# Performance work log

Measured on AMD Instinct MI355X. Metric: run time of the kernel, lower is better.

Reference implementation:

```python
import jax, jax.numpy as jnp
import numpy as np

THRESHOLD = 0.01
TOPK_RATIO = 0.7

def setup_inputs() -> dict:
    key = jax.random.key(0)
    k1, k2, k3, k4, k5 = jax.random.split(key, 5)
    B, N, F, K = 8, 2048, 512, 256
    x = jax.random.normal(k1, (B, N, F), dtype=jnp.float32)
    adj = jax.random.uniform(k2, (B, N, N), dtype=jnp.float32)
    mask = jnp.ones((B, N), dtype=jnp.float32)
    # assign_main = Linear(F->K), ReLU, Linear(K->K)
    W1 = jax.random.normal(k3, (F, K), dtype=jnp.float32) / np.sqrt(F)
    b1 = jnp.zeros((K,), dtype=jnp.float32)
    W2 = jax.random.normal(k4, (K, K), dtype=jnp.float32) / np.sqrt(K)
    b2 = jnp.zeros((K,), dtype=jnp.float32)
    return {"x": x, "adj": adj, "mask": mask, "W1": W1, "b1": b1, "W2": W2, "b2": b2}

def reference(x, adj, mask, W1, b1, W2, b2):
    B, N, Fdim = x.shape
    K = W2.shape[1]
    # soft assignment logits with masked softmax over clusters
    h = jax.nn.relu(jnp.einsum('bnf,fk->bnk', x, W1) + b1)
    logits = jnp.einsum('bnk,kl->bnl', h, W2) + b2            # [B,N,K]
    logits = logits + (-1e9) * (1.0 - mask[..., None])
    S = jax.nn.softmax(logits, axis=-1)                       # [B,N,K]
    # pooled features and pooled adjacency
    pfeat = jnp.einsum('bnk,bnf->bkf', S, x)                  # S^T x -> [B,K,F]
    mid = jnp.einsum('bnm,bmk->bnk', adj, S)                  # adj @ S
    pooled = jnp.einsum('bnk,bnl->bkl', S, mid)               # S^T adj S -> [B,K,K]
    # threshold + top-k sparsify with straight-through estimator
    topk = min(K, int(np.ceil(TOPK_RATIO * K)))
    thr_mask = (pooled >= THRESHOLD).astype(pooled.dtype)
    a_thr = pooled * thr_mask
    _, idx = jax.lax.top_k(a_thr, topk)                       # [B,K,topk]
    bi = jnp.arange(B)[:, None, None]
    ri = jnp.arange(K)[None, :, None]
    fmask = jnp.zeros_like(pooled).at[bi, ri, idx].set(1.0)
    a_sp = pooled * fmask
    a_ste = a_sp + jax.lax.stop_gradient(pooled - a_sp)       # forward == pooled
    # symmetric degree renormalization
    row_sum = a_ste.sum(axis=-1)
    d_inv_sqrt = 1.0 / jnp.sqrt(row_sum + 1e-9)
    pooled_adj = a_ste * d_inv_sqrt[:, :, None] * d_inv_sqrt[:, None, :]
    pmask = jnp.ones((B, K), dtype=x.dtype)
    return pfeat, pooled_adj, pmask
```

## Files before the change

### kernel.cpp

```cpp
#include <hip/hip_runtime.h>
#include <hip/hip_bf16.h>


typedef float f32x4 __attribute__((ext_vector_type(4)));
typedef __bf16 bf16x8 __attribute__((ext_vector_type(8)));

#define VMCNT(n) asm volatile("s_waitcnt vmcnt(" #n ")" ::: "memory")
#define LGKM0    asm volatile("s_waitcnt lgkmcnt(0)" ::: "memory")
#define SCHEDB   __builtin_amdgcn_sched_barrier(0)
#define BARRIER                                        \
  do {                                                 \
    LGKM0;                                             \
    __builtin_amdgcn_s_barrier();                      \
    asm volatile("" ::: "memory");                     \
    SCHEDB;                                            \
  } while (0)

__device__ __forceinline__ void async_load16(const void* g, void* l) {
  __builtin_amdgcn_global_load_lds((const __attribute__((address_space(1))) void*)g,
                                   (__attribute__((address_space(3))) void*)l, 16, 0, 0);
}
__device__ __forceinline__ unsigned short f2bf(float f) {
  return __builtin_bit_cast(unsigned short, (__bf16)f);
}
__device__ __forceinline__ ushort4 f4_to_bf4(float4 v) {
  ushort4 u; u.x = f2bf(v.x); u.y = f2bf(v.y); u.z = f2bf(v.z); u.w = f2bf(v.w); return u;
}

template <int ROWS, int BK, int NT>
__device__ __forceinline__ void stage_bf16(const __bf16* __restrict__ src, long long ld,
                                           __bf16* lds, int t) {
  constexpr int GR = BK / 8;
  constexpr int N = ROWS * GR / NT;
  static_assert(N >= 1, "stage too small");
#pragma unroll
  for (int c = 0; c < N; ++c) {
    const int idx = c * NT + t;
    const int row = idx / GR;
    const int g = idx % GR;
    const int gs = g ^ (row & (GR - 1) & 7);
    async_load16(src + (long long)row * ld + gs * 8, lds + idx * 8);
  }
}
template <int BK>
__device__ __forceinline__ bf16x8 frag(const __bf16* lds, int row, int kq) {
  constexpr int GR = BK / 8;
  const int g = kq ^ (row & (GR - 1) & 7);
  return *(const bf16x8*)(lds + row * BK + g * 8);
}

__global__ __launch_bounds__(256) void prep_k(const float* __restrict__ x,
                                              const float* __restrict__ W1,
                                              const float* __restrict__ W2,
                                              __bf16* __restrict__ xbT,
                                              __bf16* __restrict__ W1T,
                                              __bf16* __restrict__ W2T) {
  __shared__ float tile[64][65];
  const int tr = threadIdx.x >> 6, tc = threadIdx.x & 63;
  const int bid = blockIdx.x;
  const float* in; __bf16* out; int r0, c0, C, R;
  if (bid < 2048) {
    const int fb = bid >> 8, rest = bid & 255;
    const int nb = rest >> 3, b = rest & 7;
    in = x + (long long)b * 1048576; out = xbT + (long long)b * 1048576;
    r0 = nb * 64; c0 = fb * 64; R = 2048; C = 512;
  } else if (bid < 2080) {
    const int w = bid - 2048;
    in = W1; out = W1T; r0 = (w >> 2) * 64; c0 = (w & 3) * 64; R = 512; C = 256;
  } else {
    const int w = bid - 2080;
    in = W2; out = W2T; r0 = (w >> 2) * 64; c0 = (w & 3) * 64; R = 256; C = 256;
  }
#pragma unroll
  for (int i = 0; i < 16; ++i)
    tile[tr + i * 4][tc] = in[(long long)(r0 + tr + i * 4) * C + c0 + tc];
  __syncthreads();
#pragma unroll
  for (int i = 0; i < 16; ++i)
    out[(long long)(c0 + tr + i * 4) * R + r0 + tc] = (__bf16)tile[tc][tr + i * 4];
}

__device__ __forceinline__ void asg_compute(const __bf16* __restrict__ Abuf,
                                            const __bf16* __restrict__ Bbuf,
                                            f32x4 (&acc)[2][4], int wn, int l15, int l4) {
  bf16x8 af[2], bf[4];
#pragma unroll
  for (int i = 0; i < 2; ++i) af[i] = frag<32>(Abuf, i * 16 + l15, l4);
#pragma unroll
  for (int j = 0; j < 4; ++j) bf[j] = frag<32>(Bbuf, wn + j * 16 + l15, l4);
  __builtin_amdgcn_s_setprio(1);
#pragma unroll
  for (int i = 0; i < 2; ++i)
#pragma unroll
    for (int j = 0; j < 4; ++j)
      acc[i][j] = __builtin_amdgcn_mfma_f32_16x16x32_bf16(af[i], bf[j], acc[i][j], 0, 0, 0);
  __builtin_amdgcn_s_setprio(0);
}

__global__ __launch_bounds__(256) void assign_fused_k(
    const float* __restrict__ x, const __bf16* __restrict__ W1T,
    const __bf16* __restrict__ W2T, const float* __restrict__ b1,
    const float* __restrict__ b2, const float* __restrict__ mask,
    __bf16* __restrict__ ST) {
  __shared__ alignas(16) __bf16 Ax[2][32 * 32];
  __shared__ alignas(16) __bf16 Bw[2][256 * 32];
  __shared__ alignas(16) __bf16 hl[32 * 264];
  __shared__ float red[2][4][32];

  const int t = threadIdx.x;
  const int lane = t & 63, wave = t >> 6;
  const int l15 = lane & 15, l4 = lane >> 4;
  const int wn = wave * 64;
  const long long row0 = (long long)blockIdx.x * 32;
  const float* Xb = x + row0 * 512;

  const int arow = t >> 3, afq = t & 7;
  const int ag = afq >> 1;
  const int aoff = arow * 32 + ((ag ^ (arow & 3)) * 8) + (afq & 1) * 4;

  auto ldx = [&](int tile) -> float4 {
    return *(const float4*)(Xb + (long long)arow * 512 + tile * 32 + afq * 4);
  };
  auto sta = [&](__bf16* dst, float4 v) { *(ushort4*)&dst[aoff] = f4_to_bf4(v); };

  f32x4 acc[2][4] = {};

  float4 xA = ldx(0);
  SCHEDB;
  stage_bf16<256, 32, 256>(W1T, 512, Bw[0], t);
  SCHEDB;
  VMCNT(4); SCHEDB;
  sta(Ax[0], xA);
  float4 xB = ldx(1);
  SCHEDB;
  VMCNT(1); SCHEDB;
  BARRIER;

#pragma unroll 1
  for (int tt = 0; tt < 14; tt += 2) {
    stage_bf16<256, 32, 256>(W1T + (tt + 1) * 32, 512, Bw[1], t);
    SCHEDB;
    xA = ldx(tt + 2);
    SCHEDB;
    asg_compute(Ax[0], Bw[0], acc, wn, l15, l4);
    VMCNT(5); SCHEDB;
    sta(Ax[1], xB);
    VMCNT(1); SCHEDB;
    BARRIER;
    stage_bf16<256, 32, 256>(W1T + (tt + 2) * 32, 512, Bw[0], t);
    SCHEDB;
    xB = ldx(tt + 3);
    SCHEDB;
    asg_compute(Ax[1], Bw[1], acc, wn, l15, l4);
    VMCNT(5); SCHEDB;
    sta(Ax[0], xA);
    VMCNT(1); SCHEDB;
    BARRIER;
  }
  stage_bf16<256, 32, 256>(W1T + 15 * 32, 512, Bw[1], t);
  SCHEDB;
  asg_compute(Ax[0], Bw[0], acc, wn, l15, l4);
  VMCNT(4); SCHEDB;
  sta(Ax[1], xB);
  VMCNT(0); SCHEDB;
  BARRIER;
  asg_compute(Ax[1], Bw[1], acc, wn, l15, l4);

  stage_bf16<256, 32, 256>(W2T, 256, Bw[0], t);
  SCHEDB;
#pragma unroll
  for (int j = 0; j < 4; ++j) {
    const int col = wn + j * 16 + l15;
    const float bv = b1[col];
#pragma unroll
    for (int i = 0; i < 2; ++i)
#pragma unroll
      for (int r = 0; r < 4; ++r)
        hl[(i * 16 + l4 * 4 + r) * 264 + col] = (__bf16)fmaxf(acc[i][j][r] + bv, 0.f);
  }
  VMCNT(0); SCHEDB;
  BARRIER;

  f32x4 acc2[2][4] = {};
#pragma unroll 1
  for (int tt = 0; tt < 8; ++tt) {
    if (tt < 7) stage_bf16<256, 32, 256>(W2T + (tt + 1) * 32, 256, Bw[(tt & 1) ^ 1], t);
    SCHEDB;
    const __bf16* Bc = Bw[tt & 1];
    bf16x8 af[2], bf[4];
#pragma unroll
    for (int i = 0; i < 2; ++i)
      af[i] = *(const bf16x8*)(&hl[(i * 16 + l15) * 264 + tt * 32 + l4 * 8]);
#pragma unroll
    for (int j = 0; j < 4; ++j) bf[j] = frag<32>(Bc, wn + j * 16 + l15, l4);
#pragma unroll
    for (int i = 0; i < 2; ++i)
#pragma unroll
      for (int j = 0; j < 4; ++j)
        acc2[i][j] = __builtin_amdgcn_mfma_f32_16x16x32_bf16(af[i], bf[j], acc2[i][j], 0, 0, 0);
    VMCNT(0); SCHEDB;
    BARRIER;
  }

  float mb[2][4], mx[2][4], sm[2][4];
#pragma unroll
  for (int i = 0; i < 2; ++i)
#pragma unroll
    for (int r = 0; r < 4; ++r) {
      mb[i][r] = -1e9f * (1.0f - mask[row0 + i * 16 + l4 * 4 + r]);
      mx[i][r] = -3.4e38f;
      sm[i][r] = 0.f;
    }
#pragma unroll
  for (int j = 0; j < 4; ++j) {
    const float bv = b2[wn + j * 16 + l15];
#pragma unroll
    for (int i = 0; i < 2; ++i)
#pragma unroll
      for (int r = 0; r < 4; ++r) {
        const float v = acc2[i][j][r] + bv + mb[i][r];
        acc2[i][j][r] = v;
        mx[i][r] = fmaxf(mx[i][r], v);
      }
  }
#pragma unroll
  for (int i = 0; i < 2; ++i)
#pragma unroll
    for (int r = 0; r < 4; ++r) {
      float m = mx[i][r];
      m = fmaxf(m, __shfl_xor(m, 1, 64)); m = fmaxf(m, __shfl_xor(m, 2, 64));
      m = fmaxf(m, __shfl_xor(m, 4, 64)); m = fmaxf(m, __shfl_xor(m, 8, 64));
      mx[i][r] = m;
    }
  if (l15 == 0)
#pragma unroll
    for (int i = 0; i < 2; ++i)
#pragma unroll
      for (int r = 0; r < 4; ++r) red[0][wave][i * 16 + l4 * 4 + r] = mx[i][r];
  __syncthreads();
#pragma unroll
  for (int i = 0; i < 2; ++i)
#pragma unroll
    for (int r = 0; r < 4; ++r) {
      const int rl = i * 16 + l4 * 4 + r;
      mx[i][r] = fmaxf(fmaxf(red[0][0][rl], red[0][1][rl]),
                       fmaxf(red[0][2][rl], red[0][3][rl]));
    }
#pragma unroll
  for (int j = 0; j < 4; ++j)
#pragma unroll
    for (int i = 0; i < 2; ++i)
#pragma unroll
      for (int r = 0; r < 4; ++r) {
        const float e = __expf(acc2[i][j][r] - mx[i][r]);
        acc2[i][j][r] = e;
        sm[i][r] += e;
      }
#pragma unroll
  for (int i = 0; i < 2; ++i)
#pragma unroll
    for (int r = 0; r < 4; ++r) {
      float s = sm[i][r];
      s += __shfl_xor(s, 1, 64); s += __shfl_xor(s, 2, 64);
      s += __shfl_xor(s, 4, 64); s += __shfl_xor(s, 8, 64);
      sm[i][r] = s;
    }
  if (l15 == 0)
#pragma unroll
    for (int i = 0; i < 2; ++i)
#pragma unroll
      for (int r = 0; r < 4; ++r) red[1][wave][i * 16 + l4 * 4 + r] = sm[i][r];
  __syncthreads();
  float inv[2][4];
#pragma unroll
  for (int i = 0; i < 2; ++i)
#pragma unroll
    for (int r = 0; r < 4; ++r) {
      const int rl = i * 16 + l4 * 4 + r;
      inv[i][r] = 1.0f / (red[1][0][rl] + red[1][1][rl] + red[1][2][rl] + red[1][3][rl]);
    }
  const long long bb = row0 >> 11;
  const long long n0 = row0 & 2047;
  __bf16* Sb = ST + bb * 524288;
#pragma unroll
  for (int j = 0; j < 4; ++j) {
    const int col = wn + j * 16 + l15;
#pragma unroll
    for (int i = 0; i < 2; ++i) {
      ushort4 u;
      u.x = f2bf(acc2[i][j][0] * inv[i][0]);
      u.y = f2bf(acc2[i][j][1] * inv[i][1]);
      u.z = f2bf(acc2[i][j][2] * inv[i][2]);
      u.w = f2bf(acc2[i][j][3] * inv[i][3]);
      *(ushort4*)(Sb + (long long)col * 2048 + n0 + i * 16 + l4 * 4) = u;
    }
  }
}

__device__ __forceinline__ void adj_cmp(const __bf16* __restrict__ Abuf,
                                        const bf16x8* __restrict__ bq,
                                        f32x4 (&acc)[2][4], int l15, int l4) {
#pragma unroll
  for (int ks = 0; ks < 2; ++ks) {
    bf16x8 af[2];
#pragma unroll
    for (int i = 0; i < 2; ++i) af[i] = frag<64>(Abuf, i * 16 + l15, ks * 4 + l4);
    __builtin_amdgcn_s_setprio(1);
#pragma unroll
    for (int i = 0; i < 2; ++i)
#pragma unroll
      for (int j = 0; j < 4; ++j)
        acc[i][j] =
            __builtin_amdgcn_mfma_f32_16x16x32_bf16(af[i], bq[j * 2 + ks], acc[i][j], 0, 0, 0);
    __builtin_amdgcn_s_setprio(0);
  }
}

__global__ __launch_bounds__(256) void gemm_adj_k(const float* __restrict__ adj,
                                                  const __bf16* __restrict__ ST,
                                                  __bf16* __restrict__ midT) {
  __shared__ alignas(16) __bf16 Aa[2][32 * 64];
  const int t = threadIdx.x;
  const int lane = t & 63, wave = t >> 6;
  const int l15 = lane & 15, l4 = lane >> 4;
  const int wn = wave * 64;
  const int id = blockIdx.x;
  const int bz = id & 7;
  const long long r0 = (long long)(id >> 3) * 32;
  const float* Ab = adj + (long long)bz * 4194304 + r0 * 2048;
  const __bf16* Bb = ST + (long long)bz * 524288;

  const int arow = t >> 4, afq = t & 15;
  const int ag = afq >> 1;
  const int aoff0 = arow * 64 + ((ag ^ (arow & 7)) * 8) + (afq & 1) * 4;
  const int aoff1 = (arow + 16) * 64 + ((ag ^ ((arow + 16) & 7)) * 8) + (afq & 1) * 4;

  auto lda0 = [&](int tile) -> float4 {
    return *(const float4*)(Ab + (long long)arow * 2048 + tile * 64 + afq * 4);
  };
  auto lda1 = [&](int tile) -> float4 {
    return *(const float4*)(Ab + (long long)(arow + 16) * 2048 + tile * 64 + afq * 4);
  };
  auto sta = [&](__bf16* dst, float4 v0, float4 v1) {
    *(ushort4*)&dst[aoff0] = f4_to_bf4(v0);
    *(ushort4*)&dst[aoff1] = f4_to_bf4(v1);
  };
  auto ldb = [&](bf16x8(&dst)[8], int tile) {
#pragma unroll
    for (int j = 0; j < 4; ++j)
#pragma unroll
      for (int ks = 0; ks < 2; ++ks)
        dst[j * 2 + ks] = *(const bf16x8*)(Bb + (long long)(wn + j * 16 + l15) * 2048 +
                                           tile * 64 + ks * 32 + l4 * 8);
  };

  f32x4 acc[2][4] = {};
  bf16x8 b0[8], b1[8], b2[8];
  float4 a0_0, a0_1, a1_0, a1_1;

  a0_0 = lda0(0); a0_1 = lda1(0);
  ldb(b0, 0);
  a1_0 = lda0(1); a1_1 = lda1(1);
  ldb(b1, 1);
  SCHEDB;
  sta(Aa[0], a0_0, a0_1);
  BARRIER;

  auto step = [&](int tile, bf16x8(&bIss)[8], bf16x8(&bUse)[8],
                  float4& aI0, float4& aI1, float4& aS0, float4& aS1,
                  const __bf16* Ard, __bf16* Awr) {
    ldb(bIss, tile + 2);
    aI0 = lda0(tile + 2); aI1 = lda1(tile + 2);
    SCHEDB;
    adj_cmp(Ard, bUse, acc, l15, l4);
    sta(Awr, aS0, aS1);
    BARRIER;
  };

#pragma unroll 1
  for (int o = 0; o < 5; ++o) {
    const int base = o * 6;
    step(base + 0, b2, b0, a0_0, a0_1, a1_0, a1_1, Aa[0], Aa[1]);
    step(base + 1, b0, b1, a1_0, a1_1, a0_0, a0_1, Aa[1], Aa[0]);
    step(base + 2, b1, b2, a0_0, a0_1, a1_0, a1_1, Aa[0], Aa[1]);
    step(base + 3, b2, b0, a1_0, a1_1, a0_0, a0_1, Aa[1], Aa[0]);
    step(base + 4, b0, b1, a0_0, a0_1, a1_0, a1_1, Aa[0], Aa[1]);
    step(base + 5, b1, b2, a1_0, a1_1, a0_0, a0_1, Aa[1], Aa[0]);
  }
  adj_cmp(Aa[0], b0, acc, l15, l4);
  sta(Aa[1], a1_0, a1_1);
  BARRIER;
  adj_cmp(Aa[1], b1, acc, l15, l4);

  __bf16* Cb = midT + (long long)bz * 524288;
#pragma unroll
  for (int j = 0; j < 4; ++j) {
    const int l = wn + j * 16 + l15;
#pragma unroll
    for (int i = 0; i < 2; ++i) {
      ushort4 u;
      u.x = f2bf(acc[i][j][0]); u.y = f2bf(acc[i][j][1]);
      u.z = f2bf(acc[i][j][2]); u.w = f2bf(acc[i][j][3]);
      *(ushort4*)(Cb + (long long)l * 2048 + r0 + i * 16 + l4 * 4) = u;
    }
  }
}

__global__ __launch_bounds__(256) void gemm_feat_k(const __bf16* __restrict__ ST,
                                                   const __bf16* __restrict__ xbT,
                                                   float* __restrict__ pfeat) {
  __shared__ alignas(16) __bf16 As[3][32 * 64];
  __shared__ alignas(16) __bf16 Bs[3][64 * 64];
  const int t = threadIdx.x;
  const int lane = t & 63, wave = t >> 6;
  const int l15 = lane & 15, l4 = lane >> 4;
  const int wn = wave * 16;
  const int id = blockIdx.x;
  const int b = id & 7, j7 = id >> 3;
  const int kblk = j7 & 7, fblk = j7 >> 3;
  const __bf16* Ab = ST + (long long)b * 524288 + (long long)kblk * 32 * 2048;
  const __bf16* Bb = xbT + (long long)b * 1048576 + (long long)fblk * 64 * 2048;

  auto stage = [&](int s, int buf) {
    stage_bf16<32, 64, 256>(Ab + s * 64, 2048, (__bf16*)As + buf * 2048, t);
    stage_bf16<64, 64, 256>(Bb + s * 64, 2048, (__bf16*)Bs + buf * 4096, t);
  };
  auto cmp = [&](int buf, f32x4 (&acc)[2]) {
    const __bf16* Ac = (const __bf16*)As + buf * 2048;
    const __bf16* Bc = (const __bf16*)Bs + buf * 4096;
#pragma unroll
    for (int ks = 0; ks < 2; ++ks) {
      bf16x8 af[2], bf;
#pragma unroll
      for (int i = 0; i < 2; ++i) af[i] = frag<64>(Ac, i * 16 + l15, ks * 4 + l4);
      bf = frag<64>(Bc, wn + l15, ks * 4 + l4);
#pragma unroll
      for (int i = 0; i < 2; ++i)
        acc[i] = __builtin_amdgcn_mfma_f32_16x16x32_bf16(af[i], bf, acc[i], 0, 0, 0);
    }
  };

  f32x4 acc[2] = {};
  stage(0, 0);
  SCHEDB;
  stage(1, 1);
  SCHEDB;
  VMCNT(3); SCHEDB;
  BARRIER;

  int cur = 0, stg = 2;
#pragma unroll 1
  for (int tt = 0; tt < 30; ++tt) {
    stage(tt + 2, stg);
    SCHEDB;
    cmp(cur, acc);
    VMCNT(3); SCHEDB;
    BARRIER;
    cur = (cur == 2) ? 0 : cur + 1;
    stg = (stg == 2) ? 0 : stg + 1;
  }
  cmp(cur, acc);
  VMCNT(0); SCHEDB;
  BARRIER;
  cur = (cur == 2) ? 0 : cur + 1;
  cmp(cur, acc);

  float* out = pfeat + (long long)b * 131072;
#pragma unroll
  for (int i = 0; i < 2; ++i)
#pragma unroll
    for (int r = 0; r < 4; ++r)
      out[(long long)(kblk * 32 + i * 16 + l4 * 4 + r) * 512 + fblk * 64 + wn + l15] =
          acc[i][r];
}

__global__ __launch_bounds__(256) void gemm_pool_k(const __bf16* __restrict__ ST,
                                                   const __bf16* __restrict__ midT,
                                                   float* __restrict__ pooled) {
  __shared__ alignas(16) __bf16 As[3][32 * 64];
  __shared__ alignas(16) __bf16 Bs[3][32 * 64];
  const int t = threadIdx.x;
  const int lane = t & 63, wave = t >> 6;
  const int l15 = lane & 15, l4 = lane >> 4;
  const int wm = (wave >> 1) * 16, wn = (wave & 1) * 16;
  const int id = blockIdx.x;
  const int b = id & 7, j7 = id >> 3;
  const int kblk = j7 & 7, lblk = j7 >> 3;
  const __bf16* Ab = ST + (long long)b * 524288 + (long long)kblk * 32 * 2048;
  const __bf16* Bb = midT + (long long)b * 524288 + (long long)lblk * 32 * 2048;

  auto stage = [&](int s, int buf) {
    stage_bf16<32, 64, 256>(Ab + s * 64, 2048, (__bf16*)As + buf * 2048, t);
    stage_bf16<32, 64, 256>(Bb + s * 64, 2048, (__bf16*)Bs + buf * 2048, t);
  };
  auto cmp = [&](int buf, f32x4& acc) {
    const __bf16* Ac = (const __bf16*)As + buf * 2048;
    const __bf16* Bc = (const __bf16*)Bs + buf * 2048;
#pragma unroll
    for (int ks = 0; ks < 2; ++ks) {
      bf16x8 af = frag<64>(Ac, wm + l15, ks * 4 + l4);
      bf16x8 bf = frag<64>(Bc, wn + l15, ks * 4 + l4);
      acc = __builtin_amdgcn_mfma_f32_16x16x32_bf16(af, bf, acc, 0, 0, 0);
    }
  };

  f32x4 acc = {};
  stage(0, 0);
  SCHEDB;
  stage(1, 1);
  SCHEDB;
  VMCNT(2); SCHEDB;
  BARRIER;

  int cur = 0, stg = 2;
#pragma unroll 1
  for (int tt = 0; tt < 30; ++tt) {
    stage(tt + 2, stg);
    SCHEDB;
    cmp(cur, acc);
    VMCNT(2); SCHEDB;
    BARRIER;
    cur = (cur == 2) ? 0 : cur + 1;
    stg = (stg == 2) ? 0 : stg + 1;
  }
  cmp(cur, acc);
  VMCNT(0); SCHEDB;
  BARRIER;
  cur = (cur == 2) ? 0 : cur + 1;
  cmp(cur, acc);

  float* out = pooled + (long long)b * 65536;
#pragma unroll
  for (int r = 0; r < 4; ++r)
    out[(long long)(kblk * 32 + wm + l4 * 4 + r) * 256 + lblk * 32 + wn + l15] = acc[r];
}

__global__ __launch_bounds__(256) void rowsum_k(const float* __restrict__ pooled,
                                                float* __restrict__ dinv) {
  const int gr = blockIdx.x * 4 + (threadIdx.x >> 6);
  const int lane = threadIdx.x & 63;
  const float* p = pooled + (long long)gr * 256;
  float s = p[lane] + p[lane + 64] + p[lane + 128] + p[lane + 192];
#pragma unroll
  for (int o = 32; o > 0; o >>= 1) s += __shfl_xor(s, o, 64);
  if (lane == 0) dinv[gr] = rsqrtf(s + 1e-9f);
}

__global__ __launch_bounds__(256) void finalize_k(const float* __restrict__ pooled,
                                                  const float* __restrict__ dinv,
                                                  float* __restrict__ outAdj,
                                                  float* __restrict__ pmask) {
  const long long i = blockIdx.x * 256LL + threadIdx.x;
  const int c = (int)(i & 255);
  const int r = (int)((i >> 8) & 255);
  const int b = (int)(i >> 16);
  outAdj[i] = pooled[i] * dinv[b * 256 + r] * dinv[b * 256 + c];
  if (i < 2048) pmask[i] = 1.0f;
}

extern "C" void kernel_launch(void* const* d_in, const int* in_sizes, int n_in,
                              void* d_out, int out_size, void* d_ws, size_t ws_size,
                              hipStream_t stream) {
  (void)in_sizes; (void)n_in; (void)out_size; (void)ws_size;
  const float* x    = (const float*)d_in[0];
  const float* adj  = (const float*)d_in[1];
  const float* mask = (const float*)d_in[2];
  const float* W1   = (const float*)d_in[3];
  const float* b1   = (const float*)d_in[4];
  const float* W2   = (const float*)d_in[5];
  const float* b2   = (const float*)d_in[6];

  char* ws = (char*)d_ws;
  __bf16* ST     = (__bf16*)(ws + 0);
  __bf16* midT   = (__bf16*)(ws + 8388608);
  __bf16* xbT    = (__bf16*)(ws + 16777216);
  float*  pooled = (float*)(ws + 33554432);
  float*  dinv   = (float*)(ws + 35651584);
  __bf16* W1T    = (__bf16*)(ws + 35659776);
  __bf16* W2T    = (__bf16*)(ws + 35921920);

  float* pfeat  = (float*)d_out;
  float* outAdj = (float*)d_out + 1048576;
  float* pmask  = (float*)d_out + 1572864;

  prep_k<<<2096, 256, 0, stream>>>(x, W1, W2, xbT, W1T, W2T);
  assign_fused_k<<<512, 256, 0, stream>>>(x, W1T, W2T, b1, b2, mask, ST);
  gemm_feat_k<<<512, 256, 0, stream>>>(ST, xbT, pfeat);
  gemm_adj_k<<<512, 256, 0, stream>>>(adj, ST, midT);
  gemm_pool_k<<<512, 256, 0, stream>>>(ST, midT, pooled);
  rowsum_k<<<512, 256, 0, stream>>>(pooled, dinv);
  finalize_k<<<2048, 256, 0, stream>>>(pooled, dinv, outAdj, pmask);
}
```

Before: 138.8 us.

## Restructure adj GEMM with async LDS staging and split output columns across blocks

Rewrites gemm_adj_k to stage both the fp32 adjacency tiles (treated as raw bytes) and the S^T tiles into LDS through a three-buffer async global-to-LDS pipeline. The fp32-to-bf16 conversion now happens at fragment read time instead of through registers before the LDS store. The K=256 output dimension is split in half across blocks, doubling the grid to 1024 blocks for more parallelism. The cost is that each adjacency row tile is read twice from global memory, once per column half, which raises traffic on the kernel's largest input.

```diff
diff --git a/kernel.cpp b/kernel.cpp
--- a/kernel.cpp
+++ b/kernel.cpp
@@ -297,105 +297,80 @@
   }
 }
 
-__device__ __forceinline__ void adj_cmp(const __bf16* __restrict__ Abuf,
-                                        const bf16x8* __restrict__ bq,
-                                        f32x4 (&acc)[2][4], int l15, int l4) {
-#pragma unroll
-  for (int ks = 0; ks < 2; ++ks) {
-    bf16x8 af[2];
-#pragma unroll
-    for (int i = 0; i < 2; ++i) af[i] = frag<64>(Abuf, i * 16 + l15, ks * 4 + l4);
-    __builtin_amdgcn_s_setprio(1);
-#pragma unroll
-    for (int i = 0; i < 2; ++i)
-#pragma unroll
-      for (int j = 0; j < 4; ++j)
-        acc[i][j] =
-            __builtin_amdgcn_mfma_f32_16x16x32_bf16(af[i], bq[j * 2 + ks], acc[i][j], 0, 0, 0);
-    __builtin_amdgcn_s_setprio(0);
-  }
-}
-
 __global__ __launch_bounds__(256) void gemm_adj_k(const float* __restrict__ adj,
                                                   const __bf16* __restrict__ ST,
                                                   __bf16* __restrict__ midT) {
-  __shared__ alignas(16) __bf16 Aa[2][32 * 64];
+  __shared__ alignas(16) __bf16 As[3][32 * 64];
+  __shared__ alignas(16) __bf16 Bs[3][128 * 32];
   const int t = threadIdx.x;
   const int lane = t & 63, wave = t >> 6;
   const int l15 = lane & 15, l4 = lane >> 4;
-  const int wn = wave * 64;
+  const int wn = wave * 32;
   const int id = blockIdx.x;
   const int bz = id & 7;
-  const long long r0 = (long long)(id >> 3) * 32;
-  const float* Ab = adj + (long long)bz * 4194304 + r0 * 2048;
-  const __bf16* Bb = ST + (long long)bz * 524288;
-
-  const int arow = t >> 4, afq = t & 15;
-  const int ag = afq >> 1;
-  const int aoff0 = arow * 64 + ((ag ^ (arow & 7)) * 8) + (afq & 1) * 4;
-  const int aoff1 = (arow + 16) * 64 + ((ag ^ ((arow + 16) & 7)) * 8) + (afq & 1) * 4;
-
-  auto lda0 = [&](int tile) -> float4 {
-    return *(const float4*)(Ab + (long long)arow * 2048 + tile * 64 + afq * 4);
-  };
-  auto lda1 = [&](int tile) -> float4 {
-    return *(const float4*)(Ab + (long long)(arow + 16) * 2048 + tile * 64 + afq * 4);
-  };
-  auto sta = [&](__bf16* dst, float4 v0, float4 v1) {
-    *(ushort4*)&dst[aoff0] = f4_to_bf4(v0);
-    *(ushort4*)&dst[aoff1] = f4_to_bf4(v1);
-  };
-  auto ldb = [&](bf16x8(&dst)[8], int tile) {
-#pragma unroll
-    for (int j = 0; j < 4; ++j)
-#pragma unroll
-      for (int ks = 0; ks < 2; ++ks)
-        dst[j * 2 + ks] = *(const bf16x8*)(Bb + (long long)(wn + j * 16 + l15) * 2048 +
-                                           tile * 64 + ks * 32 + l4 * 8);
-  };
-
-  f32x4 acc[2][4] = {};
-  bf16x8 b0[8], b1[8], b2[8];
-  float4 a0_0, a0_1, a1_0, a1_1;
-
-  a0_0 = lda0(0); a0_1 = lda1(0);
-  ldb(b0, 0);
-  a1_0 = lda0(1); a1_1 = lda1(1);
-  ldb(b1, 1);
-  SCHEDB;
-  sta(Aa[0], a0_0, a0_1);
-  BARRIER;
-
-  auto step = [&](int tile, bf16x8(&bIss)[8], bf16x8(&bUse)[8],
-                  float4& aI0, float4& aI1, float4& aS0, float4& aS1,
-                  const __bf16* Ard, __bf16* Awr) {
-    ldb(bIss, tile + 2);
-    aI0 = lda0(tile + 2); aI1 = lda1(tile + 2);
-    SCHEDB;
-    adj_cmp(Ard, bUse, acc, l15, l4);
-    sta(Awr, aS0, aS1);
+  const int nh = (id >> 3) & 1;
+  const long long r0 = (long long)(id >> 4) * 32;
+  const __bf16* Abh = (const __bf16*)(adj + (long long)bz * 4194304 + r0 * 2048);
+  const __bf16* Bb = ST + (long long)bz * 524288 + (long long)nh * 128 * 2048;
+
+  auto stage = [&](int s, int buf) {
+    stage_bf16<32, 64, 256>(Abh + s * 64, 4096, (__bf16*)As + buf * 2048, t);
+    stage_bf16<128, 32, 256>(Bb + s * 32, 2048, (__bf16*)Bs + buf * 4096, t);
+  };
+  auto afrag = [&](const __bf16* Ac, int row) {
+    f32x4 lo = __builtin_bit_cast(f32x4, frag<64>(Ac, row, l4 * 2));
+    f32x4 hi = __builtin_bit_cast(f32x4, frag<64>(Ac, row, l4 * 2 + 1));
+    bf16x8 r;
+    r[0] = (__bf16)lo[0]; r[1] = (__bf16)lo[1]; r[2] = (__bf16)lo[2]; r[3] = (__bf16)lo[3];
+    r[4] = (__bf16)hi[0]; r[5] = (__bf16)hi[1]; r[6] = (__bf16)hi[2]; r[7] = (__bf16)hi[3];
+    return r;
+  };
+  f32x4 acc[2][2] = {};
+  auto cmp = [&](int buf) {
+    const __bf16* Ac = (const __bf16*)As + buf * 2048;
+    const __bf16* Bc = (const __bf16*)Bs + buf * 4096;
+    bf16x8 af[2], bf[2];
+#pragma unroll
+    for (int i = 0; i < 2; ++i) af[i] = afrag(Ac, i * 16 + l15);
+#pragma unroll
+    for (int j = 0; j < 2; ++j) bf[j] = frag<32>(Bc, wn + j * 16 + l15, l4);
+    __builtin_amdgcn_s_setprio(1);
+#pragma unroll
+    for (int i = 0; i < 2; ++i)
+#pragma unroll
+      for (int j = 0; j < 2; ++j)
+        acc[i][j] = __builtin_amdgcn_mfma_f32_16x16x32_bf16(af[i], bf[j], acc[i][j], 0, 0, 0);
+    __builtin_amdgcn_s_setprio(0);
+  };
+
+  stage(0, 0);
+  SCHEDB;
+  stage(1, 1);
+  SCHEDB;
+  VMCNT(3); SCHEDB;
+  BARRIER;
+
+  int cur = 0, stg = 2;
+#pragma unroll 1
+  for (int tt = 0; tt < 62; ++tt) {
+    stage(tt + 2, stg);
+    SCHEDB;
+    cmp(cur);
+    VMCNT(3); SCHEDB;
     BARRIER;
-  };
-
-#pragma unroll 1
-  for (int o = 0; o < 5; ++o) {
-    const int base = o * 6;
-    step(base + 0, b2, b0, a0_0, a0_1, a1_0, a1_1, Aa[0], Aa[1]);
-    step(base + 1, b0, b1, a1_0, a1_1, a0_0, a0_1, Aa[1], Aa[0]);
-    step(base + 2, b1, b2, a0_0, a0_1, a1_0, a1_1, Aa[0], Aa[1]);
-    step(base + 3, b2, b0, a1_0, a1_1, a0_0, a0_1, Aa[1], Aa[0]);
-    step(base + 4, b0, b1, a0_0, a0_1, a1_0, a1_1, Aa[0], Aa[1]);
-    step(base + 5, b1, b2, a1_0, a1_1, a0_0, a0_1, Aa[1], Aa[0]);
-  }
-  adj_cmp(Aa[0], b0, acc, l15, l4);
-  sta(Aa[1], a1_0, a1_1);
-  BARRIER;
-  adj_cmp(Aa[1], b1, acc, l15, l4);
+    cur = (cur == 2) ? 0 : cur + 1;
+    stg = (stg == 2) ? 0 : stg + 1;
+  }
+  cmp(cur);
+  VMCNT(0); SCHEDB;
+  BARRIER;
+  cur = (cur == 2) ? 0 : cur + 1;
+  cmp(cur);
 
   __bf16* Cb = midT + (long long)bz * 524288;
 #pragma unroll
-  for (int j = 0; j < 4; ++j) {
-    const int l = wn + j * 16 + l15;
+  for (int j = 0; j < 2; ++j) {
+    const int l = nh * 128 + wn + j * 16 + l15;
 #pragma unroll
     for (int i = 0; i < 2; ++i) {
       ushort4 u;
@@ -586,7 +561,7 @@
   prep_k<<<2096, 256, 0, stream>>>(x, W1, W2, xbT, W1T, W2T);
   assign_fused_k<<<512, 256, 0, stream>>>(x, W1T, W2T, b1, b2, mask, ST);
   gemm_feat_k<<<512, 256, 0, stream>>>(ST, xbT, pfeat);
-  gemm_adj_k<<<512, 256, 0, stream>>>(adj, ST, midT);
+  gemm_adj_k<<<1024, 256, 0, stream>>>(adj, ST, midT);
   gemm_pool_k<<<512, 256, 0, stream>>>(ST, midT, pooled);
   rowsum_k<<<512, 256, 0, stream>>>(pooled, dinv);
   finalize_k<<<2048, 256, 0, stream>>>(pooled, dinv, outAdj, pmask);
```

Measured after the change: 123.6 us. 10.9% less time.
